# Kernel optimization log

Hardware: AMD Instinct MI355X
Metric: run time of the kernel (lower is better)

Reference implementation:

```python
import jax, jax.numpy as jnp
import numpy as np

N = 50000
EPS_BN = 1e-5
NEG_SLOPE = 0.2


def _gat_layer(x, src, dst, W, a_src, a_dst, b):
    # x: [N, in], W: [in, H*C], a_src/a_dst: [H, C], b: [C]
    H, C = a_src.shape
    h = (x @ W).reshape(N, H, C)                      # [N,H,C]
    s = jnp.einsum('nhc,hc->nh', h, a_src)            # per-node src score
    d = jnp.einsum('nhc,hc->nh', h, a_dst)            # per-node dst score
    e = jax.nn.leaky_relu(s[src] + d[dst], NEG_SLOPE)  # [E,H]
    # segment softmax over edges sharing the same destination node
    emax = jax.ops.segment_max(e, dst, num_segments=N)
    emax = jnp.where(jnp.isfinite(emax), emax, 0.0)
    ex = jnp.exp(e - emax[dst])
    denom = jax.ops.segment_sum(ex, dst, num_segments=N)
    alpha = ex / (denom[dst] + 1e-16)                 # [E,H]
    msg = h[src] * alpha[:, :, None]                  # [E,H,C] (dominant tensor)
    out = jax.ops.segment_sum(msg, dst, num_segments=N)  # [N,H,C]
    return out.mean(axis=1) + b                       # concat=False -> head mean


def _batch_norm(y, gamma, beta):
    mu = y.mean(axis=0)
    var = y.var(axis=0)
    return (y - mu) * jax.lax.rsqrt(var + EPS_BN) * gamma + beta


def setup_inputs() -> dict:
    key = jax.random.key(0)
    ks = jax.random.split(key, 20)
    in_dim, hid, heads = 256, 128, 4
    E = 400000
    x = jax.random.normal(ks[0], (N, in_dim), dtype=jnp.float32)
    edge_index = jax.random.randint(ks[1], (2, E), 0, N, dtype=jnp.int64)
    def glorot(k, shape):
        fan = shape[0] + shape[-1]
        return jax.random.normal(k, shape, dtype=jnp.float32) * np.sqrt(2.0 / fan)
    inp = {'x': x, 'edge_index': edge_index}
    # layer 0: 256 -> 128, H=4 ; layer 1: 128 -> 128, H=4 ; layer 2: 128 -> 128, H=1
    dims = [(in_dim, hid, heads), (hid, hid, heads), (hid, hid, 1)]
    for i, (ci, co, h) in enumerate(dims):
        inp[f'W{i}'] = glorot(ks[2 + 5 * i], (ci, h * co))
        inp[f'a_src{i}'] = glorot(ks[3 + 5 * i], (h, co))
        inp[f'a_dst{i}'] = glorot(ks[4 + 5 * i], (h, co))
        inp[f'b{i}'] = jnp.zeros((co,), dtype=jnp.float32)
        inp[f'gamma{i}'] = jnp.ones((co,), dtype=jnp.float32)
        inp[f'beta{i}'] = jnp.zeros((co,), dtype=jnp.float32)
    return inp


def reference(x, edge_index,
              W0, a_src0, a_dst0, b0, gamma0, beta0,
              W1, a_src1, a_dst1, b1, gamma1, beta1,
              W2, a_src2, a_dst2, b2, gamma2, beta2):
    # add self-loops once (GATConv default add_self_loops=True, same every layer)
    loops = jnp.arange(N, dtype=edge_index.dtype)
    src = jnp.concatenate([edge_index[0], loops])
    dst = jnp.concatenate([edge_index[1], loops])
    params = [(W0, a_src0, a_dst0, b0, gamma0, beta0),
              (W1, a_src1, a_dst1, b1, gamma1, beta1),
              (W2, a_src2, a_dst2, b2, gamma2, beta2)]
    h = x
    for i, (W, asr, ads, b, g, be) in enumerate(params):
        h = _gat_layer(h, src, dst, W, asr, ads, b)
        h = _batch_norm(h, g, be)
        if i < len(params) - 1:
            h = jax.nn.relu(h)  # dropout is identity in eval mode
    return h
```

## Files before the change

kernel.cpp:

```cpp
#include <hip/hip_runtime.h>
#include <cstdint>
#include <cstddef>

#define N_NODES 50000
#define M_PAD   50176
#define EPS_BN  1e-5f
#define NEG     0.2f

typedef __attribute__((ext_vector_type(8))) short bf16x8;
typedef __attribute__((ext_vector_type(4))) float f32x4;

static __device__ __forceinline__ ushort f2bf(float f) {
    unsigned u = __float_as_uint(f);
    unsigned r = (u + 0x7FFFu + ((u >> 16) & 1u)) >> 16;
    return (ushort)r;
}
static __device__ __forceinline__ float bf2f(ushort b) {
    return __uint_as_float(((unsigned)b) << 16);
}
static __device__ __forceinline__ float leaky(float v) {
    return (v > 0.f) ? v : NEG * v;
}
static __device__ __forceinline__ void wave_fence() {
    __builtin_amdgcn_fence(__ATOMIC_ACQ_REL, "wavefront");
}

__global__ __launch_bounds__(256) void prep(
    const float* __restrict__ x, ushort* __restrict__ Xbf,
    const float* __restrict__ W0, const float* __restrict__ W1,
    const float* __restrict__ W2, ushort* __restrict__ Wt0,
    ushort* __restrict__ Wt1, ushort* __restrict__ Wt2) {
    const int gi = blockIdx.x * 256 + threadIdx.x;
    const int e0 = gi * 4;
    if (e0 < M_PAD * 256) {
        const int row = e0 >> 8;
        ushort4 o;
        if (row < N_NODES) {
            const float4 v = *(const float4*)&x[e0];
            o = make_ushort4(f2bf(v.x), f2bf(v.y), f2bf(v.z), f2bf(v.w));
        } else {
            o = make_ushort4(0, 0, 0, 0);
        }
        *(ushort4*)&Xbf[e0] = o;
    }
    if (gi < 131072) {
        const int k = gi >> 9, n = gi & 511;
        Wt0[(size_t)n * 256 + k] = f2bf(W0[gi]);
    } else if (gi < 196608) {
        const int j = gi - 131072;
        const int k = j >> 9, n = j & 511;
        Wt1[(size_t)n * 128 + k] = f2bf(W1[j]);
    } else if (gi < 212992) {
        const int j = gi - 196608;
        const int k = j >> 7, n = j & 127;
        Wt2[(size_t)n * 128 + k] = f2bf(W2[j]);
    }
}

__global__ __launch_bounds__(256) void gemm_bf(
    const ushort* __restrict__ A, const ushort* __restrict__ Bt,
    ushort* __restrict__ C, int K, int Nc) {
    __shared__ ushort As[128 * 32];
    __shared__ ushort Bs[64 * 32];
    const int t = threadIdx.x;
    const int wave = t >> 6, lane = t & 63;
    const int quad = lane >> 4, l16 = lane & 15;
    const int m0 = blockIdx.y * 128, n0 = blockIdx.x * 64;

    const int aRow = t >> 2, aCol = (t & 3) * 8;
    const ushort* aG0 = A + (size_t)(m0 + aRow) * K + aCol;
    const ushort* aG1 = A + (size_t)(m0 + 64 + aRow) * K + aCol;
    const ushort* bG  = Bt + (size_t)(n0 + aRow) * K + aCol;

    const int aOff0 = (wave * 32 + l16) * 32 + quad * 8;
    const int aOff1 = aOff0 + 16 * 32;
    const int bOff  = l16 * 32 + quad * 8;

    f32x4 acc[2][4] = {};
    for (int k0 = 0; k0 < K; k0 += 32) {
        const uint4 a0 = *(const uint4*)(aG0 + k0);
        const uint4 a1 = *(const uint4*)(aG1 + k0);
        const uint4 b0 = *(const uint4*)(bG + k0);
        __syncthreads();
        *(uint4*)&As[t * 8]        = a0;
        *(uint4*)&As[2048 + t * 8] = a1;
        *(uint4*)&Bs[t * 8]        = b0;
        __syncthreads();
        const bf16x8 af0 = *(const bf16x8*)&As[aOff0];
        const bf16x8 af1 = *(const bf16x8*)&As[aOff1];
#pragma unroll
        for (int nt = 0; nt < 4; ++nt) {
            const bf16x8 bf = *(const bf16x8*)&Bs[bOff + nt * 512];
            acc[0][nt] = __builtin_amdgcn_mfma_f32_16x16x32_bf16(af0, bf, acc[0][nt], 0, 0, 0);
            acc[1][nt] = __builtin_amdgcn_mfma_f32_16x16x32_bf16(af1, bf, acc[1][nt], 0, 0, 0);
        }
    }
    const int rowBase = m0 + wave * 32;
#pragma unroll
    for (int mt = 0; mt < 2; ++mt) {
#pragma unroll
        for (int nt = 0; nt < 4; ++nt) {
            const int col = n0 + nt * 16 + l16;
#pragma unroll
            for (int r = 0; r < 4; ++r) {
                const int row = rowBase + mt * 16 + quad * 4 + r;
                C[(size_t)row * Nc + col] = f2bf(acc[mt][nt][r]);
            }
        }
    }
}

__global__ __launch_bounds__(256) void gemm_bn(
    const float* __restrict__ Y, const float* __restrict__ stats,
    const ushort* __restrict__ Bt, ushort* __restrict__ C, int Nc) {
    constexpr int K = 128;
    __shared__ ushort As[128 * 32];
    __shared__ ushort Bs[64 * 32];
    __shared__ float lsc[128], lsh[128];
    const int t = threadIdx.x;
    if (t < 128) { lsc[t] = stats[t]; lsh[t] = stats[128 + t]; }
    const int wave = t >> 6, lane = t & 63;
    const int quad = lane >> 4, l16 = lane & 15;
    const int m0 = blockIdx.y * 128, n0 = blockIdx.x * 64;

    const int aRow = t >> 2, aCol = (t & 3) * 8;
    const float* yG0 = Y + (size_t)(m0 + aRow) * K + aCol;
    const float* yG1 = Y + (size_t)(m0 + 64 + aRow) * K + aCol;
    const ushort* bG = Bt + (size_t)(n0 + aRow) * K + aCol;

    const int aOff0 = (wave * 32 + l16) * 32 + quad * 8;
    const int aOff1 = aOff0 + 16 * 32;
    const int bOff  = l16 * 32 + quad * 8;

    f32x4 acc[2][4] = {};
    for (int k0 = 0; k0 < K; k0 += 32) {
        const float4 a00 = *(const float4*)(yG0 + k0);
        const float4 a01 = *(const float4*)(yG0 + k0 + 4);
        const float4 a10 = *(const float4*)(yG1 + k0);
        const float4 a11 = *(const float4*)(yG1 + k0 + 4);
        const uint4 b0 = *(const uint4*)(bG + k0);
        __syncthreads();
        const int c = aCol + k0;
        ushort u0[8], u1[8];
        u0[0] = f2bf(fmaxf(a00.x * lsc[c+0] + lsh[c+0], 0.f));
        u0[1] = f2bf(fmaxf(a00.y * lsc[c+1] + lsh[c+1], 0.f));
        u0[2] = f2bf(fmaxf(a00.z * lsc[c+2] + lsh[c+2], 0.f));
        u0[3] = f2bf(fmaxf(a00.w * lsc[c+3] + lsh[c+3], 0.f));
        u0[4] = f2bf(fmaxf(a01.x * lsc[c+4] + lsh[c+4], 0.f));
        u0[5] = f2bf(fmaxf(a01.y * lsc[c+5] + lsh[c+5], 0.f));
        u0[6] = f2bf(fmaxf(a01.z * lsc[c+6] + lsh[c+6], 0.f));
        u0[7] = f2bf(fmaxf(a01.w * lsc[c+7] + lsh[c+7], 0.f));
        u1[0] = f2bf(fmaxf(a10.x * lsc[c+0] + lsh[c+0], 0.f));
        u1[1] = f2bf(fmaxf(a10.y * lsc[c+1] + lsh[c+1], 0.f));
        u1[2] = f2bf(fmaxf(a10.z * lsc[c+2] + lsh[c+2], 0.f));
        u1[3] = f2bf(fmaxf(a10.w * lsc[c+3] + lsh[c+3], 0.f));
        u1[4] = f2bf(fmaxf(a11.x * lsc[c+4] + lsh[c+4], 0.f));
        u1[5] = f2bf(fmaxf(a11.y * lsc[c+5] + lsh[c+5], 0.f));
        u1[6] = f2bf(fmaxf(a11.z * lsc[c+6] + lsh[c+6], 0.f));
        u1[7] = f2bf(fmaxf(a11.w * lsc[c+7] + lsh[c+7], 0.f));
        *(uint4*)&As[t * 8]        = *(uint4*)u0;
        *(uint4*)&As[2048 + t * 8] = *(uint4*)u1;
        *(uint4*)&Bs[t * 8]        = b0;
        __syncthreads();
        const bf16x8 af0 = *(const bf16x8*)&As[aOff0];
        const bf16x8 af1 = *(const bf16x8*)&As[aOff1];
#pragma unroll
        for (int nt = 0; nt < 4; ++nt) {
            const bf16x8 bf = *(const bf16x8*)&Bs[bOff + nt * 512];
            acc[0][nt] = __builtin_amdgcn_mfma_f32_16x16x32_bf16(af0, bf, acc[0][nt], 0, 0, 0);
            acc[1][nt] = __builtin_amdgcn_mfma_f32_16x16x32_bf16(af1, bf, acc[1][nt], 0, 0, 0);
        }
    }
    const int rowBase = m0 + wave * 32;
#pragma unroll
    for (int mt = 0; mt < 2; ++mt) {
#pragma unroll
        for (int nt = 0; nt < 4; ++nt) {
            const int col = n0 + nt * 16 + l16;
#pragma unroll
            for (int r = 0; r < 4; ++r) {
                const int row = rowBase + mt * 16 + quad * 4 + r;
                C[(size_t)row * Nc + col] = f2bf(acc[mt][nt][r]);
            }
        }
    }
}

template <int H>
__global__ __launch_bounds__(128) void scores_kernel(
    const ushort* __restrict__ h, const float* __restrict__ a_src,
    const float* __restrict__ a_dst, float* __restrict__ s,
    float* __restrict__ d) {
    const int n = blockIdx.x, t = threadIdx.x;
    if (t < 32 * H) {
        const int head = t >> 5;
        const int c0 = (t & 31) * 4;
        const ushort4 hv = *(const ushort4*)&h[(size_t)n * (H * 128) + head * 128 + c0];
        const float4 as = *(const float4*)&a_src[head * 128 + c0];
        const float4 ad = *(const float4*)&a_dst[head * 128 + c0];
        const float h0 = bf2f(hv.x), h1 = bf2f(hv.y), h2 = bf2f(hv.z), h3 = bf2f(hv.w);
        float ps = h0 * as.x + h1 * as.y + h2 * as.z + h3 * as.w;
        float pd = h0 * ad.x + h1 * ad.y + h2 * ad.z + h3 * ad.w;
#pragma unroll
        for (int m = 16; m >= 1; m >>= 1) {
            ps += __shfl_xor(ps, m, 32);
            pd += __shfl_xor(pd, m, 32);
        }
        if ((t & 31) == 0) {
            s[n * H + head] = ps;
            d[n * H + head] = pd;
        }
    }
}

__global__ void edge_hist(const int* __restrict__ ei, int E, int* __restrict__ cnt) {
    const int k = blockIdx.x * blockDim.x + threadIdx.x;
    const int ET = E + N_NODES;
    if (k < ET) {
        const int dstn = (k < E) ? ei[E + k] : (k - E);
        atomicAdd(&cnt[dstn], 1);
    }
}

__global__ __launch_bounds__(256) void scan_phase1(
    const int* __restrict__ cnt, int* __restrict__ incl,
    int* __restrict__ bsum, int n) {
    __shared__ int sh[256];
    const int b = blockIdx.x, t = threadIdx.x;
    const int i0 = b * 1024 + t * 4;
    int v[4]; int sum = 0;
#pragma unroll
    for (int k = 0; k < 4; ++k) {
        v[k] = (i0 + k < n) ? cnt[i0 + k] : 0;
        sum += v[k];
    }
    sh[t] = sum;
    __syncthreads();
    for (int off = 1; off < 256; off <<= 1) {
        const int a = (t >= off) ? sh[t - off] : 0;
        __syncthreads();
        sh[t] += a;
        __syncthreads();
    }
    int run = sh[t] - sum;
#pragma unroll
    for (int k = 0; k < 4; ++k) {
        run += v[k];
        if (i0 + k < n) incl[i0 + k] = run;
    }
    if (t == 255) bsum[b] = sh[255];
}

__global__ void scan_phase3b(const int* __restrict__ incl, const int* __restrict__ bsum,
                             int* __restrict__ rowptr, int* __restrict__ cursor, int n) {
    __shared__ int P[2];
    const int b = blockIdx.x;
    const int gA = (b * 256) >> 10;
    if (threadIdx.x == 0) {
        int p = 0;
        for (int k = 0; k < gA; ++k) p += bsum[k];
        P[0] = p;
        P[1] = (gA > 0) ? (p - bsum[gA - 1]) : 0;
    }
    __syncthreads();
    const int i = b * 256 + threadIdx.x;
    if (i < n) {
        rowptr[i + 1] = incl[i] + P[0];
        if (i == 0) cursor[0] = 0;
        else cursor[i] = incl[i - 1] + ((((i - 1) >> 10) == gA) ? P[0] : P[1]);
    }
    if (i == 0) rowptr[0] = 0;
}

__global__ void edge_scatter(const int* __restrict__ ei, int E,
                             int* __restrict__ cursor, int* __restrict__ col) {
    const int k = blockIdx.x * blockDim.x + threadIdx.x;
    const int ET = E + N_NODES;
    if (k < ET) {
        const int srcn = (k < E) ? ei[k] : (k - E);
        const int dstn = (k < E) ? ei[E + k] : (k - E);
        const int p = atomicAdd(&cursor[dstn], 1);
        col[p] = srcn;
    }
}

__global__ __launch_bounds__(256, 8) void aggregate4(
    const ushort* __restrict__ h, const float* __restrict__ s,
    const float* __restrict__ d, const int* __restrict__ rowptr,
    const int* __restrict__ col, const float* __restrict__ bias,
    float* __restrict__ y) {
    __shared__ int   ls[4][128];
    __shared__ float lex[4][512];
    const int t = threadIdx.x, w = t >> 6, lane = t & 63;
    const int n = blockIdx.x * 4 + w;
    const int head = lane >> 4;
    const int rs = rowptr[n], re = rowptr[n + 1], deg = re - rs;
    const float4 dn = *(const float4*)&d[n * 4];
    int* lsw = ls[w];
    float* lexw = lex[w];

    float acc[8];
#pragma unroll
    for (int k = 0; k < 8; ++k) acc[k] = 0.f;
    float4 dsum = make_float4(0.f, 0.f, 0.f, 0.f);
    float4 mx = make_float4(-3.4e38f, -3.4e38f, -3.4e38f, -3.4e38f);

    if (deg <= 128) {
#pragma unroll
        for (int it = 0; it < 2; ++it) {
            const int jj = lane + it * 64;
            if (jj < deg) {
                const int sn = col[rs + jj];
                lsw[jj] = sn;
                const float4 sv = *(const float4*)&s[sn * 4];
                float4 e;
                e.x = leaky(sv.x + dn.x); e.y = leaky(sv.y + dn.y);
                e.z = leaky(sv.z + dn.z); e.w = leaky(sv.w + dn.w);
                *(float4*)&lexw[jj * 4] = e;
                mx.x = fmaxf(mx.x, e.x); mx.y = fmaxf(mx.y, e.y);
                mx.z = fmaxf(mx.z, e.z); mx.w = fmaxf(mx.w, e.w);
            }
        }
#pragma unroll
        for (int off = 1; off < 64; off <<= 1) {
            mx.x = fmaxf(mx.x, __shfl_xor(mx.x, off));
            mx.y = fmaxf(mx.y, __shfl_xor(mx.y, off));
            mx.z = fmaxf(mx.z, __shfl_xor(mx.z, off));
            mx.w = fmaxf(mx.w, __shfl_xor(mx.w, off));
        }
#pragma unroll
        for (int it = 0; it < 2; ++it) {
            const int jj = lane + it * 64;
            if (jj < deg) {
                float4 e = *(const float4*)&lexw[jj * 4];
                e.x = __expf(e.x - mx.x); e.y = __expf(e.y - mx.y);
                e.z = __expf(e.z - mx.z); e.w = __expf(e.w - mx.w);
                *(float4*)&lexw[jj * 4] = e;
                dsum.x += e.x; dsum.y += e.y; dsum.z += e.z; dsum.w += e.w;
            }
        }
        wave_fence();
        int jj = 0;
        for (; jj + 2 <= deg; jj += 2) {
            const int sn0 = lsw[jj], sn1 = lsw[jj + 1];
            const float e0 = lexw[jj * 4 + head];
            const float e1 = lexw[(jj + 1) * 4 + head];
            const bf16x8 hv0 = *(const bf16x8*)&h[(size_t)sn0 * 512 + lane * 8];
            const bf16x8 hv1 = *(const bf16x8*)&h[(size_t)sn1 * 512 + lane * 8];
#pragma unroll
            for (int k = 0; k < 8; ++k) {
                acc[k] = fmaf(e0, bf2f((ushort)hv0[k]), acc[k]);
                acc[k] = fmaf(e1, bf2f((ushort)hv1[k]), acc[k]);
            }
        }
        if (jj < deg) {
            const int sn = lsw[jj];
            const float e0 = lexw[jj * 4 + head];
            const bf16x8 hv = *(const bf16x8*)&h[(size_t)sn * 512 + lane * 8];
#pragma unroll
            for (int k = 0; k < 8; ++k) acc[k] = fmaf(e0, bf2f((ushort)hv[k]), acc[k]);
        }
    } else {
        for (int j = rs + lane; j < re; j += 64) {
            const float4 sv = *(const float4*)&s[col[j] * 4];
            mx.x = fmaxf(mx.x, leaky(sv.x + dn.x));
            mx.y = fmaxf(mx.y, leaky(sv.y + dn.y));
            mx.z = fmaxf(mx.z, leaky(sv.z + dn.z));
            mx.w = fmaxf(mx.w, leaky(sv.w + dn.w));
        }
#pragma unroll
        for (int off = 1; off < 64; off <<= 1) {
            mx.x = fmaxf(mx.x, __shfl_xor(mx.x, off));
            mx.y = fmaxf(mx.y, __shfl_xor(mx.y, off));
            mx.z = fmaxf(mx.z, __shfl_xor(mx.z, off));
            mx.w = fmaxf(mx.w, __shfl_xor(mx.w, off));
        }
        for (int c0 = rs; c0 < re; c0 += 128) {
            const int cend = min(re, c0 + 128);
#pragma unroll
            for (int it = 0; it < 2; ++it) {
                const int j = c0 + lane + it * 64;
                if (j < cend) {
                    const int sn = col[j];
                    const int jj = j - c0;
                    lsw[jj] = sn;
                    const float4 sv = *(const float4*)&s[sn * 4];
                    float4 e;
                    e.x = __expf(leaky(sv.x + dn.x) - mx.x);
                    e.y = __expf(leaky(sv.y + dn.y) - mx.y);
                    e.z = __expf(leaky(sv.z + dn.z) - mx.z);
                    e.w = __expf(leaky(sv.w + dn.w) - mx.w);
                    *(float4*)&lexw[jj * 4] = e;
                    dsum.x += e.x; dsum.y += e.y; dsum.z += e.z; dsum.w += e.w;
                }
            }
            wave_fence();
            const int cnum = cend - c0;
            for (int jj = 0; jj < cnum; ++jj) {
                const int sn = lsw[jj];
                const float exh = lexw[jj * 4 + head];
                const bf16x8 hv = *(const bf16x8*)&h[(size_t)sn * 512 + lane * 8];
#pragma unroll
                for (int k = 0; k < 8; ++k) acc[k] = fmaf(exh, bf2f((ushort)hv[k]), acc[k]);
            }
            wave_fence();
        }
    }

#pragma unroll
    for (int off = 1; off < 64; off <<= 1) {
        dsum.x += __shfl_xor(dsum.x, off);
        dsum.y += __shfl_xor(dsum.y, off);
        dsum.z += __shfl_xor(dsum.z, off);
        dsum.w += __shfl_xor(dsum.w, off);
    }
    const float dsel = (head == 0) ? dsum.x : (head == 1) ? dsum.y
                     : (head == 2) ? dsum.z : dsum.w;
    const float inv = 1.f / (dsel + 1e-16f);
    wave_fence();
#pragma unroll
    for (int k = 0; k < 8; ++k) lexw[lane * 8 + k] = acc[k] * inv;
    wave_fence();
    {
        const int c = lane * 2;
        const float m0 = 0.25f * (lexw[c] + lexw[128 + c] + lexw[256 + c] + lexw[384 + c]);
        const float m1 = 0.25f * (lexw[c + 1] + lexw[128 + c + 1] + lexw[256 + c + 1] + lexw[384 + c + 1]);
        float2 o = make_float2(m0 + bias[c], m1 + bias[c + 1]);
        *(float2*)&y[(size_t)n * 128 + c] = o;
    }
}

__global__ __launch_bounds__(256, 8) void aggregate1(
    const ushort* __restrict__ h, const float* __restrict__ s,
    const float* __restrict__ d, const int* __restrict__ rowptr,
    const int* __restrict__ col, const float* __restrict__ bias,
    float* __restrict__ y) {
    __shared__ int   ls[4][128];
    __shared__ float lex[4][128];
    const int t = threadIdx.x, w = t >> 6, lane = t & 63;
    const int n = blockIdx.x * 4 + w;
    const int rs = rowptr[n], re = rowptr[n + 1], deg = re - rs;
    const float dn = d[n];
    int* lsw = ls[w];
    float* lexw = lex[w];

    float acc0 = 0.f, acc1 = 0.f, dsum = 0.f;
    float mx = -3.4e38f;

    if (deg <= 128) {
#pragma unroll
        for (int it = 0; it < 2; ++it) {
            const int jj = lane + it * 64;
            if (jj < deg) {
                const int sn = col[rs + jj];
                lsw[jj] = sn;
                const float e = leaky(s[sn] + dn);
                lexw[jj] = e;
                mx = fmaxf(mx, e);
            }
        }
#pragma unroll
        for (int off = 1; off < 64; off <<= 1) mx = fmaxf(mx, __shfl_xor(mx, off));
#pragma unroll
        for (int it = 0; it < 2; ++it) {
            const int jj = lane + it * 64;
            if (jj < deg) {
                const float ex = __expf(lexw[jj] - mx);
                lexw[jj] = ex;
                dsum += ex;
            }
        }
        wave_fence();
        int jj = 0;
        for (; jj + 2 <= deg; jj += 2) {
            const int sn0 = lsw[jj], sn1 = lsw[jj + 1];
            const float e0 = lexw[jj], e1 = lexw[jj + 1];
            const ushort2 hv0 = *(const ushort2*)&h[(size_t)sn0 * 128 + lane * 2];
            const ushort2 hv1 = *(const ushort2*)&h[(size_t)sn1 * 128 + lane * 2];
            acc0 = fmaf(e0, bf2f(hv0.x), acc0); acc1 = fmaf(e0, bf2f(hv0.y), acc1);
            acc0 = fmaf(e1, bf2f(hv1.x), acc0); acc1 = fmaf(e1, bf2f(hv1.y), acc1);
        }
        if (jj < deg) {
            const int sn = lsw[jj];
            const float ex = lexw[jj];
            const ushort2 hv = *(const ushort2*)&h[(size_t)sn * 128 + lane * 2];
            acc0 = fmaf(ex, bf2f(hv.x), acc0);
            acc1 = fmaf(ex, bf2f(hv.y), acc1);
        }
    } else {
        for (int j = rs + lane; j < re; j += 64) {
            mx = fmaxf(mx, leaky(s[col[j]] + dn));
        }
#pragma unroll
        for (int off = 1; off < 64; off <<= 1) mx = fmaxf(mx, __shfl_xor(mx, off));
        for (int c0 = rs; c0 < re; c0 += 128) {
            const int cend = min(re, c0 + 128);
#pragma unroll
            for (int it = 0; it < 2; ++it) {
                const int j = c0 + lane + it * 64;
                if (j < cend) {
                    const int sn = col[j];
                    const int jj = j - c0;
                    lsw[jj] = sn;
                    const float ex = __expf(leaky(s[sn] + dn) - mx);
                    lexw[jj] = ex;
                    dsum += ex;
                }
            }
            wave_fence();
            const int cnum = cend - c0;
            for (int jj = 0; jj < cnum; ++jj) {
                const int sn = lsw[jj];
                const float ex = lexw[jj];
                const ushort2 hv = *(const ushort2*)&h[(size_t)sn * 128 + lane * 2];
                acc0 = fmaf(ex, bf2f(hv.x), acc0);
                acc1 = fmaf(ex, bf2f(hv.y), acc1);
            }
            wave_fence();
        }
    }
#pragma unroll
    for (int off = 1; off < 64; off <<= 1) dsum += __shfl_xor(dsum, off);
    const float inv = 1.f / (dsum + 1e-16f);
    const int c = lane * 2;
    float2 o = make_float2(acc0 * inv + bias[c], acc1 * inv + bias[c + 1]);
    *(float2*)&y[(size_t)n * 128 + c] = o;
}

__global__ __launch_bounds__(256) void bn_stats_fused(
    const float* __restrict__ y, float* __restrict__ partial,
    const float* __restrict__ gamma, const float* __restrict__ beta,
    float* __restrict__ stats, unsigned* __restrict__ ticket) {
    const int b = blockIdx.x, t = threadIdx.x;
    const int c = t & 127;
    float sum = 0.f, sq = 0.f;
    for (int r = b * 2 + (t >> 7); r < N_NODES; r += 512) {
        const float v = y[(size_t)r * 128 + c];
        sum += v;
        sq += v * v;
    }
    __shared__ float s1[256], s2[256];
    s1[t] = sum; s2[t] = sq;
    __syncthreads();
    if (t < 128) {
        partial[(size_t)b * 256 + c] = s1[t] + s1[t + 128];
        partial[(size_t)b * 256 + 128 + c] = s2[t] + s2[t + 128];
    }
    __threadfence();
    __shared__ unsigned rank;
    if (t == 0) rank = atomicAdd(ticket, 1u);
    __syncthreads();
    if (rank == 255u) {
        __threadfence();
        if (t < 128) {
            float S = 0.f, Q = 0.f;
            for (int b2 = 0; b2 < 256; ++b2) {
                S += partial[(size_t)b2 * 256 + t];
                Q += partial[(size_t)b2 * 256 + 128 + t];
            }
            const float mu = S / (float)N_NODES;
            const float var = Q / (float)N_NODES - mu * mu;
            const float sc = gamma[t] * rsqrtf(var + EPS_BN);
            stats[t] = sc;
            stats[128 + t] = beta[t] - mu * sc;
        }
    }
}

__global__ void bn_apply_out(const float* __restrict__ y,
                             const float* __restrict__ stats,
                             float* __restrict__ out) {
    const int i = blockIdx.x * blockDim.x + threadIdx.x;
    if (i < N_NODES * 128) {
        const int c = i & 127;
        out[i] = y[i] * stats[c] + stats[128 + c];
    }
}

extern "C" void kernel_launch(void* const* d_in, const int* in_sizes, int n_in,
                              void* d_out, int out_size, void* d_ws, size_t ws_size,
                              hipStream_t stream) {
    const float* x = (const float*)d_in[0];
    const int* ei = (const int*)d_in[1];
    const int E = in_sizes[1] / 2;
    const int ET = E + N_NODES;

    const float* W[3]    = {(const float*)d_in[2], (const float*)d_in[8],  (const float*)d_in[14]};
    const float* ASRC[3] = {(const float*)d_in[3], (const float*)d_in[9],  (const float*)d_in[15]};
    const float* ADST[3] = {(const float*)d_in[4], (const float*)d_in[10], (const float*)d_in[16]};
    const float* BIAS[3] = {(const float*)d_in[5], (const float*)d_in[11], (const float*)d_in[17]};
    const float* GAM[3]  = {(const float*)d_in[6], (const float*)d_in[12], (const float*)d_in[18]};
    const float* BET[3]  = {(const float*)d_in[7], (const float*)d_in[13], (const float*)d_in[19]};

    char* base = (char*)d_ws;
    auto alloc = [&](size_t bytes) {
        char* p = base;
        base += (bytes + 255) & ~(size_t)255;
        return p;
    };
    ushort* hbf    = (ushort*)alloc((size_t)M_PAD * 512 * 2);
    ushort* Xbf    = (ushort*)alloc((size_t)M_PAD * 256 * 2);
    ushort* Wt0    = (ushort*)alloc((size_t)512 * 256 * 2);
    ushort* Wt1    = (ushort*)alloc((size_t)512 * 128 * 2);
    ushort* Wt2    = (ushort*)alloc((size_t)128 * 128 * 2);
    float*  y      = (float*)alloc((size_t)M_PAD * 128 * 4);
    float*  s      = (float*)alloc((size_t)N_NODES * 4 * 4);
    float*  dsc    = (float*)alloc((size_t)N_NODES * 4 * 4);
    int*    rowptr = (int*)alloc((size_t)(N_NODES + 1) * 4);
    int*    col    = (int*)alloc((size_t)ET * 4);
    int*    cnt    = (int*)alloc((size_t)(N_NODES + 8) * 4);
    int*    incl   = (int*)alloc((size_t)N_NODES * 4);
    int*    bsum   = (int*)alloc((size_t)64 * 4);
    float*  partial = (float*)alloc((size_t)256 * 256 * 4);
    float*  stats   = (float*)alloc((size_t)256 * 4);
    if ((size_t)(base - (char*)d_ws) > ws_size) return;

    unsigned* tickets = (unsigned*)(cnt + N_NODES);

    const int eb = (ET + 255) / 256;
    const int nScanB = (N_NODES + 1023) / 1024;

    hipMemsetAsync(cnt, 0, (size_t)(N_NODES + 8) * 4, stream);
    edge_hist<<<eb, 256, 0, stream>>>(ei, E, cnt);
    scan_phase1<<<nScanB, 256, 0, stream>>>(cnt, incl, bsum, N_NODES);
    scan_phase3b<<<(N_NODES + 255) / 256, 256, 0, stream>>>(incl, bsum, rowptr, cnt, N_NODES);
    edge_scatter<<<eb, 256, 0, stream>>>(ei, E, cnt, col);

    prep<<<(M_PAD * 256 / 4 + 255) / 256, 256, 0, stream>>>(
        x, Xbf, W[0], W[1], W[2], Wt0, Wt1, Wt2);

    {
        dim3 g0(512 / 64, M_PAD / 128);
        gemm_bf<<<g0, 256, 0, stream>>>(Xbf, Wt0, hbf, 256, 512);
        scores_kernel<4><<<N_NODES, 128, 0, stream>>>(hbf, ASRC[0], ADST[0], s, dsc);
        aggregate4<<<N_NODES / 4, 256, 0, stream>>>(hbf, s, dsc, rowptr, col, BIAS[0], y);
        bn_stats_fused<<<256, 256, 0, stream>>>(y, partial, GAM[0], BET[0], stats, tickets + 0);
    }
    {
        dim3 g1(512 / 64, M_PAD / 128);
        gemm_bn<<<g1, 256, 0, stream>>>(y, stats, Wt1, hbf, 512);
        scores_kernel<4><<<N_NODES, 128, 0, stream>>>(hbf, ASRC[1], ADST[1], s, dsc);
        aggregate4<<<N_NODES / 4, 256, 0, stream>>>(hbf, s, dsc, rowptr, col, BIAS[1], y);
        bn_stats_fused<<<256, 256, 0, stream>>>(y, partial, GAM[1], BET[1], stats, tickets + 1);
    }
    {
        dim3 g2(128 / 64, M_PAD / 128);
        gemm_bn<<<g2, 256, 0, stream>>>(y, stats, Wt2, hbf, 128);
        scores_kernel<1><<<N_NODES, 128, 0, stream>>>(hbf, ASRC[2], ADST[2], s, dsc);
        aggregate1<<<N_NODES / 4, 256, 0, stream>>>(hbf, s, dsc, rowptr, col, BIAS[2], y);
        bn_stats_fused<<<256, 256, 0, stream>>>(y, partial, GAM[2], BET[2], stats, tickets + 2);
    }
    bn_apply_out<<<(N_NODES * 128 + 255) / 256, 256, 0, stream>>>(y, stats, (float*)d_out);
}
```

Measured before the change: 640.3 us.

## Fuse attention score computation into GEMM epilogue and merge histogram into prep

Result: faster. 571.1 us (-10.8%).

```diff
diff --git a/kernel.cpp b/kernel.cpp
--- a/kernel.cpp
+++ b/kernel.cpp
@@ -29,7 +29,8 @@
     const float* __restrict__ x, ushort* __restrict__ Xbf,
     const float* __restrict__ W0, const float* __restrict__ W1,
     const float* __restrict__ W2, ushort* __restrict__ Wt0,
-    ushort* __restrict__ Wt1, ushort* __restrict__ Wt2) {
+    ushort* __restrict__ Wt1, ushort* __restrict__ Wt2,
+    const int* __restrict__ ei, int E, int* __restrict__ cnt) {
     const int gi = blockIdx.x * 256 + threadIdx.x;
     const int e0 = gi * 4;
     if (e0 < M_PAD * 256) {
@@ -55,51 +56,103 @@
         const int k = j >> 7, n = j & 127;
         Wt2[(size_t)n * 128 + k] = f2bf(W2[j]);
     }
-}
-
-__global__ __launch_bounds__(256) void gemm_bf(
-    const ushort* __restrict__ A, const ushort* __restrict__ Bt,
-    ushort* __restrict__ C, int K, int Nc) {
+    const int ET = E + N_NODES;
+    if (gi < ET) {
+        const int dstn = (gi < E) ? ei[E + gi] : (gi - E);
+        atomicAdd(&cnt[dstn], 1);
+    }
+}
+
+template <bool BNIN>
+__global__ __launch_bounds__(256, 4) void gemm_fused(
+    const ushort* __restrict__ Abf, const float* __restrict__ Y,
+    const float* __restrict__ stats, const ushort* __restrict__ Bt,
+    ushort* __restrict__ C, int K, int Nc, int H,
+    const float* __restrict__ a_src, const float* __restrict__ a_dst,
+    float* __restrict__ s, float* __restrict__ d) {
     __shared__ ushort As[128 * 32];
-    __shared__ ushort Bs[64 * 32];
+    __shared__ ushort Bs[128 * 32];
+    __shared__ float lsc[128], lsh[128];
     const int t = threadIdx.x;
+    if (BNIN && t < 128) { lsc[t] = stats[t]; lsh[t] = stats[128 + t]; }
     const int wave = t >> 6, lane = t & 63;
     const int quad = lane >> 4, l16 = lane & 15;
-    const int m0 = blockIdx.y * 128, n0 = blockIdx.x * 64;
+    const int m0 = blockIdx.y * 128, n0 = blockIdx.x * 128;
+    const int hd = n0 >> 7;
 
     const int aRow = t >> 2, aCol = (t & 3) * 8;
-    const ushort* aG0 = A + (size_t)(m0 + aRow) * K + aCol;
-    const ushort* aG1 = A + (size_t)(m0 + 64 + aRow) * K + aCol;
-    const ushort* bG  = Bt + (size_t)(n0 + aRow) * K + aCol;
+    const ushort* aG0 = Abf + (size_t)(m0 + aRow) * K + aCol;
+    const ushort* aG1 = Abf + (size_t)(m0 + 64 + aRow) * K + aCol;
+    const float*  yG0 = Y + (size_t)(m0 + aRow) * 128 + aCol;
+    const float*  yG1 = Y + (size_t)(m0 + 64 + aRow) * 128 + aCol;
+    const ushort* bG0 = Bt + (size_t)(n0 + aRow) * K + aCol;
+    const ushort* bG1 = Bt + (size_t)(n0 + 64 + aRow) * K + aCol;
 
     const int aOff0 = (wave * 32 + l16) * 32 + quad * 8;
     const int aOff1 = aOff0 + 16 * 32;
-    const int bOff  = l16 * 32 + quad * 8;
-
-    f32x4 acc[2][4] = {};
+
+    f32x4 acc[2][8] = {};
     for (int k0 = 0; k0 < K; k0 += 32) {
-        const uint4 a0 = *(const uint4*)(aG0 + k0);
-        const uint4 a1 = *(const uint4*)(aG1 + k0);
-        const uint4 b0 = *(const uint4*)(bG + k0);
-        __syncthreads();
-        *(uint4*)&As[t * 8]        = a0;
-        *(uint4*)&As[2048 + t * 8] = a1;
-        *(uint4*)&Bs[t * 8]        = b0;
+        uint4 sa0, sa1;
+        if constexpr (BNIN) {
+            const float4 a00 = *(const float4*)(yG0 + k0);
+            const float4 a01 = *(const float4*)(yG0 + k0 + 4);
+            const float4 a10 = *(const float4*)(yG1 + k0);
+            const float4 a11 = *(const float4*)(yG1 + k0 + 4);
+            const int c = aCol + k0;
+            __syncthreads();
+            ushort u0[8], u1[8];
+            u0[0] = f2bf(fmaxf(a00.x * lsc[c+0] + lsh[c+0], 0.f));
+            u0[1] = f2bf(fmaxf(a00.y * lsc[c+1] + lsh[c+1], 0.f));
+            u0[2] = f2bf(fmaxf(a00.z * lsc[c+2] + lsh[c+2], 0.f));
+            u0[3] = f2bf(fmaxf(a00.w * lsc[c+3] + lsh[c+3], 0.f));
+            u0[4] = f2bf(fmaxf(a01.x * lsc[c+4] + lsh[c+4], 0.f));
+            u0[5] = f2bf(fmaxf(a01.y * lsc[c+5] + lsh[c+5], 0.f));
+            u0[6] = f2bf(fmaxf(a01.z * lsc[c+6] + lsh[c+6], 0.f));
+            u0[7] = f2bf(fmaxf(a01.w * lsc[c+7] + lsh[c+7], 0.f));
+            u1[0] = f2bf(fmaxf(a10.x * lsc[c+0] + lsh[c+0], 0.f));
+            u1[1] = f2bf(fmaxf(a10.y * lsc[c+1] + lsh[c+1], 0.f));
+            u1[2] = f2bf(fmaxf(a10.z * lsc[c+2] + lsh[c+2], 0.f));
+            u1[3] = f2bf(fmaxf(a10.w * lsc[c+3] + lsh[c+3], 0.f));
+            u1[4] = f2bf(fmaxf(a11.x * lsc[c+4] + lsh[c+4], 0.f));
+            u1[5] = f2bf(fmaxf(a11.y * lsc[c+5] + lsh[c+5], 0.f));
+            u1[6] = f2bf(fmaxf(a11.z * lsc[c+6] + lsh[c+6], 0.f));
+            u1[7] = f2bf(fmaxf(a11.w * lsc[c+7] + lsh[c+7], 0.f));
+            sa0 = *(uint4*)u0;
+            sa1 = *(uint4*)u1;
+            const uint4 b0 = *(const uint4*)(bG0 + k0);
+            const uint4 b1 = *(const uint4*)(bG1 + k0);
+            *(uint4*)&As[t * 8]        = sa0;
+            *(uint4*)&As[2048 + t * 8] = sa1;
+            *(uint4*)&Bs[t * 8]        = b0;
+            *(uint4*)&Bs[2048 + t * 8] = b1;
+        } else {
+            sa0 = *(const uint4*)(aG0 + k0);
+            sa1 = *(const uint4*)(aG1 + k0);
+            const uint4 b0 = *(const uint4*)(bG0 + k0);
+            const uint4 b1 = *(const uint4*)(bG1 + k0);
+            __syncthreads();
+            *(uint4*)&As[t * 8]        = sa0;
+            *(uint4*)&As[2048 + t * 8] = sa1;
+            *(uint4*)&Bs[t * 8]        = b0;
+            *(uint4*)&Bs[2048 + t * 8] = b1;
+        }
         __syncthreads();
         const bf16x8 af0 = *(const bf16x8*)&As[aOff0];
         const bf16x8 af1 = *(const bf16x8*)&As[aOff1];
 #pragma unroll
-        for (int nt = 0; nt < 4; ++nt) {
-            const bf16x8 bf = *(const bf16x8*)&Bs[bOff + nt * 512];
+        for (int nt = 0; nt < 8; ++nt) {
+            const bf16x8 bf = *(const bf16x8*)&Bs[(nt * 16 + l16) * 32 + quad * 8];
             acc[0][nt] = __builtin_amdgcn_mfma_f32_16x16x32_bf16(af0, bf, acc[0][nt], 0, 0, 0);
             acc[1][nt] = __builtin_amdgcn_mfma_f32_16x16x32_bf16(af1, bf, acc[1][nt], 0, 0, 0);
         }
     }
+
     const int rowBase = m0 + wave * 32;
 #pragma unroll
     for (int mt = 0; mt < 2; ++mt) {
 #pragma unroll
-        for (int nt = 0; nt < 4; ++nt) {
+        for (int nt = 0; nt < 8; ++nt) {
             const int col = n0 + nt * 16 + l16;
 #pragma unroll
             for (int r = 0; r < 4; ++r) {
@@ -108,117 +161,47 @@
             }
         }
     }
-}
-
-__global__ __launch_bounds__(256) void gemm_bn(
-    const float* __restrict__ Y, const float* __restrict__ stats,
-    const ushort* __restrict__ Bt, ushort* __restrict__ C, int Nc) {
-    constexpr int K = 128;
-    __shared__ ushort As[128 * 32];
-    __shared__ ushort Bs[64 * 32];
-    __shared__ float lsc[128], lsh[128];
-    const int t = threadIdx.x;
-    if (t < 128) { lsc[t] = stats[t]; lsh[t] = stats[128 + t]; }
-    const int wave = t >> 6, lane = t & 63;
-    const int quad = lane >> 4, l16 = lane & 15;
-    const int m0 = blockIdx.y * 128, n0 = blockIdx.x * 64;
-
-    const int aRow = t >> 2, aCol = (t & 3) * 8;
-    const float* yG0 = Y + (size_t)(m0 + aRow) * K + aCol;
-    const float* yG1 = Y + (size_t)(m0 + 64 + aRow) * K + aCol;
-    const ushort* bG = Bt + (size_t)(n0 + aRow) * K + aCol;
-
-    const int aOff0 = (wave * 32 + l16) * 32 + quad * 8;
-    const int aOff1 = aOff0 + 16 * 32;
-    const int bOff  = l16 * 32 + quad * 8;
-
-    f32x4 acc[2][4] = {};
-    for (int k0 = 0; k0 < K; k0 += 32) {
-        const float4 a00 = *(const float4*)(yG0 + k0);
-        const float4 a01 = *(const float4*)(yG0 + k0 + 4);
-        const float4 a10 = *(const float4*)(yG1 + k0);
-        const float4 a11 = *(const float4*)(yG1 + k0 + 4);
-        const uint4 b0 = *(const uint4*)(bG + k0);
-        __syncthreads();
-        const int c = aCol + k0;
-        ushort u0[8], u1[8];
-        u0[0] = f2bf(fmaxf(a00.x * lsc[c+0] + lsh[c+0], 0.f));
-        u0[1] = f2bf(fmaxf(a00.y * lsc[c+1] + lsh[c+1], 0.f));
-        u0[2] = f2bf(fmaxf(a00.z * lsc[c+2] + lsh[c+2], 0.f));
-        u0[3] = f2bf(fmaxf(a00.w * lsc[c+3] + lsh[c+3], 0.f));
-        u0[4] = f2bf(fmaxf(a01.x * lsc[c+4] + lsh[c+4], 0.f));
-        u0[5] = f2bf(fmaxf(a01.y * lsc[c+5] + lsh[c+5], 0.f));
-        u0[6] = f2bf(fmaxf(a01.z * lsc[c+6] + lsh[c+6], 0.f));
-        u0[7] = f2bf(fmaxf(a01.w * lsc[c+7] + lsh[c+7], 0.f));
-        u1[0] = f2bf(fmaxf(a10.x * lsc[c+0] + lsh[c+0], 0.f));
-        u1[1] = f2bf(fmaxf(a10.y * lsc[c+1] + lsh[c+1], 0.f));
-        u1[2] = f2bf(fmaxf(a10.z * lsc[c+2] + lsh[c+2], 0.f));
-        u1[3] = f2bf(fmaxf(a10.w * lsc[c+3] + lsh[c+3], 0.f));
-        u1[4] = f2bf(fmaxf(a11.x * lsc[c+4] + lsh[c+4], 0.f));
-        u1[5] = f2bf(fmaxf(a11.y * lsc[c+5] + lsh[c+5], 0.f));
-        u1[6] = f2bf(fmaxf(a11.z * lsc[c+6] + lsh[c+6], 0.f));
-        u1[7] = f2bf(fmaxf(a11.w * lsc[c+7] + lsh[c+7], 0.f));
-        *(uint4*)&As[t * 8]        = *(uint4*)u0;
-        *(uint4*)&As[2048 + t * 8] = *(uint4*)u1;
-        *(uint4*)&Bs[t * 8]        = b0;
-        __syncthreads();
-        const bf16x8 af0 = *(const bf16x8*)&As[aOff0];
-        const bf16x8 af1 = *(const bf16x8*)&As[aOff1];
-#pragma unroll
-        for (int nt = 0; nt < 4; ++nt) {
-            const bf16x8 bf = *(const bf16x8*)&Bs[bOff + nt * 512];
-            acc[0][nt] = __builtin_amdgcn_mfma_f32_16x16x32_bf16(af0, bf, acc[0][nt], 0, 0, 0);
-            acc[1][nt] = __builtin_amdgcn_mfma_f32_16x16x32_bf16(af1, bf, acc[1][nt], 0, 0, 0);
-        }
-    }
-    const int rowBase = m0 + wave * 32;
-#pragma unroll
-    for (int mt = 0; mt < 2; ++mt) {
-#pragma unroll
-        for (int nt = 0; nt < 4; ++nt) {
-            const int col = n0 + nt * 16 + l16;
+
+    float aS[8], aD[8];
+#pragma unroll
+    for (int nt = 0; nt < 8; ++nt) {
+        aS[nt] = a_src[hd * 128 + nt * 16 + l16];
+        aD[nt] = a_dst[hd * 128 + nt * 16 + l16];
+    }
+    float ps[2][4], pd[2][4];
+#pragma unroll
+    for (int mt = 0; mt < 2; ++mt)
+#pragma unroll
+        for (int r = 0; r < 4; ++r) {
+            float vs = 0.f, vd = 0.f;
+#pragma unroll
+            for (int nt = 0; nt < 8; ++nt) {
+                vs = fmaf(acc[mt][nt][r], aS[nt], vs);
+                vd = fmaf(acc[mt][nt][r], aD[nt], vd);
+            }
+            ps[mt][r] = vs; pd[mt][r] = vd;
+        }
+#pragma unroll
+    for (int off = 1; off < 16; off <<= 1) {
+#pragma unroll
+        for (int mt = 0; mt < 2; ++mt)
+#pragma unroll
+            for (int r = 0; r < 4; ++r) {
+                ps[mt][r] += __shfl_xor(ps[mt][r], off);
+                pd[mt][r] += __shfl_xor(pd[mt][r], off);
+            }
+    }
+    if (l16 == 0) {
+#pragma unroll
+        for (int mt = 0; mt < 2; ++mt)
 #pragma unroll
             for (int r = 0; r < 4; ++r) {
                 const int row = rowBase + mt * 16 + quad * 4 + r;
-                C[(size_t)row * Nc + col] = f2bf(acc[mt][nt][r]);
-            }
-        }
-    }
-}
-
-template <int H>
-__global__ __launch_bounds__(128) void scores_kernel(
-    const ushort* __restrict__ h, const float* __restrict__ a_src,
-    const float* __restrict__ a_dst, float* __restrict__ s,
-    float* __restrict__ d) {
-    const int n = blockIdx.x, t = threadIdx.x;
-    if (t < 32 * H) {
-        const int head = t >> 5;
-        const int c0 = (t & 31) * 4;
-        const ushort4 hv = *(const ushort4*)&h[(size_t)n * (H * 128) + head * 128 + c0];
-        const float4 as = *(const float4*)&a_src[head * 128 + c0];
-        const float4 ad = *(const float4*)&a_dst[head * 128 + c0];
-        const float h0 = bf2f(hv.x), h1 = bf2f(hv.y), h2 = bf2f(hv.z), h3 = bf2f(hv.w);
-        float ps = h0 * as.x + h1 * as.y + h2 * as.z + h3 * as.w;
-        float pd = h0 * ad.x + h1 * ad.y + h2 * ad.z + h3 * ad.w;
-#pragma unroll
-        for (int m = 16; m >= 1; m >>= 1) {
-            ps += __shfl_xor(ps, m, 32);
-            pd += __shfl_xor(pd, m, 32);
-        }
-        if ((t & 31) == 0) {
-            s[n * H + head] = ps;
-            d[n * H + head] = pd;
-        }
-    }
-}
-
-__global__ void edge_hist(const int* __restrict__ ei, int E, int* __restrict__ cnt) {
-    const int k = blockIdx.x * blockDim.x + threadIdx.x;
-    const int ET = E + N_NODES;
-    if (k < ET) {
-        const int dstn = (k < E) ? ei[E + k] : (k - E);
-        atomicAdd(&cnt[dstn], 1);
+                if (row < N_NODES) {
+                    s[row * H + hd] = ps[mt][r];
+                    d[row * H + hd] = pd[mt][r];
+                }
+            }
     }
 }
 
@@ -341,19 +324,26 @@
         }
         wave_fence();
         int jj = 0;
-        for (; jj + 2 <= deg; jj += 2) {
+        for (; jj + 4 <= deg; jj += 4) {
             const int sn0 = lsw[jj], sn1 = lsw[jj + 1];
+            const int sn2 = lsw[jj + 2], sn3 = lsw[jj + 3];
             const float e0 = lexw[jj * 4 + head];
             const float e1 = lexw[(jj + 1) * 4 + head];
+            const float e2 = lexw[(jj + 2) * 4 + head];
+            const float e3 = lexw[(jj + 3) * 4 + head];
             const bf16x8 hv0 = *(const bf16x8*)&h[(size_t)sn0 * 512 + lane * 8];
             const bf16x8 hv1 = *(const bf16x8*)&h[(size_t)sn1 * 512 + lane * 8];
+            const bf16x8 hv2 = *(const bf16x8*)&h[(size_t)sn2 * 512 + lane * 8];
+            const bf16x8 hv3 = *(const bf16x8*)&h[(size_t)sn3 * 512 + lane * 8];
 #pragma unroll
             for (int k = 0; k < 8; ++k) {
                 acc[k] = fmaf(e0, bf2f((ushort)hv0[k]), acc[k]);
                 acc[k] = fmaf(e1, bf2f((ushort)hv1[k]), acc[k]);
-            }
-        }
-        if (jj < deg) {
+                acc[k] = fmaf(e2, bf2f((ushort)hv2[k]), acc[k]);
+                acc[k] = fmaf(e3, bf2f((ushort)hv3[k]), acc[k]);
+            }
+        }
+        for (; jj < deg; ++jj) {
             const int sn = lsw[jj];
             const float e0 = lexw[jj * 4 + head];
             const bf16x8 hv = *(const bf16x8*)&h[(size_t)sn * 512 + lane * 8];
@@ -472,15 +462,21 @@
         }
         wave_fence();
         int jj = 0;
-        for (; jj + 2 <= deg; jj += 2) {
+        for (; jj + 4 <= deg; jj += 4) {
             const int sn0 = lsw[jj], sn1 = lsw[jj + 1];
+            const int sn2 = lsw[jj + 2], sn3 = lsw[jj + 3];
             const float e0 = lexw[jj], e1 = lexw[jj + 1];
+            const float e2 = lexw[jj + 2], e3 = lexw[jj + 3];
             const ushort2 hv0 = *(const ushort2*)&h[(size_t)sn0 * 128 + lane * 2];
             const ushort2 hv1 = *(const ushort2*)&h[(size_t)sn1 * 128 + lane * 2];
+            const ushort2 hv2 = *(const ushort2*)&h[(size_t)sn2 * 128 + lane * 2];
+            const ushort2 hv3 = *(const ushort2*)&h[(size_t)sn3 * 128 + lane * 2];
             acc0 = fmaf(e0, bf2f(hv0.x), acc0); acc1 = fmaf(e0, bf2f(hv0.y), acc1);
             acc0 = fmaf(e1, bf2f(hv1.x), acc0); acc1 = fmaf(e1, bf2f(hv1.y), acc1);
-        }
-        if (jj < deg) {
+            acc0 = fmaf(e2, bf2f(hv2.x), acc0); acc1 = fmaf(e2, bf2f(hv2.y), acc1);
+            acc0 = fmaf(e3, bf2f(hv3.x), acc0); acc1 = fmaf(e3, bf2f(hv3.y), acc1);
+        }
+        for (; jj < deg; ++jj) {
             const int sn = lsw[jj];
             const float ex = lexw[jj];
             const ushort2 hv = *(const ushort2*)&h[(size_t)sn * 128 + lane * 2];
@@ -621,32 +617,30 @@
     const int nScanB = (N_NODES + 1023) / 1024;
 
     hipMemsetAsync(cnt, 0, (size_t)(N_NODES + 8) * 4, stream);
-    edge_hist<<<eb, 256, 0, stream>>>(ei, E, cnt);
+    prep<<<(M_PAD * 256 / 4 + 255) / 256, 256, 0, stream>>>(
+        x, Xbf, W[0], W[1], W[2], Wt0, Wt1, Wt2, ei, E, cnt);
     scan_phase1<<<nScanB, 256, 0, stream>>>(cnt, incl, bsum, N_NODES);
     scan_phase3b<<<(N_NODES + 255) / 256, 256, 0, stream>>>(incl, bsum, rowptr, cnt, N_NODES);
     edge_scatter<<<eb, 256, 0, stream>>>(ei, E, cnt, col);
 
-    prep<<<(M_PAD * 256 / 4 + 255) / 256, 256, 0, stream>>>(
-        x, Xbf, W[0], W[1], W[2], Wt0, Wt1, Wt2);
-
     {
-        dim3 g0(512 / 64, M_PAD / 128);
-        gemm_bf<<<g0, 256, 0, stream>>>(Xbf, Wt0, hbf, 256, 512);
-        scores_kernel<4><<<N_NODES, 128, 0, stream>>>(hbf, ASRC[0], ADST[0], s, dsc);
+        dim3 g0(512 / 128, M_PAD / 128);
+        gemm_fused<false><<<g0, 256, 0, stream>>>(
+            Xbf, nullptr, nullptr, Wt0, hbf, 256, 512, 4, ASRC[0], ADST[0], s, dsc);
         aggregate4<<<N_NODES / 4, 256, 0, stream>>>(hbf, s, dsc, rowptr, col, BIAS[0], y);
         bn_stats_fused<<<256, 256, 0, stream>>>(y, partial, GAM[0], BET[0], stats, tickets + 0);
     }
     {
-        dim3 g1(512 / 64, M_PAD / 128);
-        gemm_bn<<<g1, 256, 0, stream>>>(y, stats, Wt1, hbf, 512);
-        scores_kernel<4><<<N_NODES, 128, 0, stream>>>(hbf, ASRC[1], ADST[1], s, dsc);
+        dim3 g1(512 / 128, M_PAD / 128);
+        gemm_fused<true><<<g1, 256, 0, stream>>>(
+            nullptr, y, stats, Wt1, hbf, 128, 512, 4, ASRC[1], ADST[1], s, dsc);
         aggregate4<<<N_NODES / 4, 256, 0, stream>>>(hbf, s, dsc, rowptr, col, BIAS[1], y);
         bn_stats_fused<<<256, 256, 0, stream>>>(y, partial, GAM[1], BET[1], stats, tickets + 1);
     }
     {
-        dim3 g2(128 / 64, M_PAD / 128);
-        gemm_bn<<<g2, 256, 0, stream>>>(y, stats, Wt2, hbf, 128);
-        scores_kernel<1><<<N_NODES, 128, 0, stream>>>(hbf, ASRC[2], ADST[2], s, dsc);
+        dim3 g2(128 / 128, M_PAD / 128);
+        gemm_fused<true><<<g2, 256, 0, stream>>>(
+            nullptr, y, stats, Wt2, hbf, 128, 128, 1, ASRC[2], ADST[2], s, dsc);
         aggregate1<<<N_NODES / 4, 256, 0, stream>>>(hbf, s, dsc, rowptr, col, BIAS[2], y);
         bn_stats_fused<<<256, 256, 0, stream>>>(y, partial, GAM[2], BET[2], stats, tickets + 2);
     }
```
